# Kernel tuning notes

Measured on AMD Instinct MI355X. Metric: run time of the kernel, lower is better.

Reference implementation:

```python
import jax, jax.numpy as jnp
import numpy as np

# ---- module hyperparameters (init_kwargs) ----
FRAME_PERIOD = 120
SAMPLE_RATE = 24000
FFT_LENGTH = 2048
DEFAULT_F0 = 500.0
Q1 = -0.15
F_MIN = 3.0 * SAMPLE_RATE / (FFT_LENGTH - 3)
EPS_SAFE = 1e-12                      # safeguard noise inside windowing (WORLD kMySafeGuardMinimum)
EPS_F32 = float(np.finfo(np.float32).eps)  # torch.finfo(x.dtype).eps
TAU = 2.0 * np.pi
MAX_F0_STATIC = 600.0                 # static bound on f0 for the smoothing mirror pad
K_PAD = int(MAX_F0_STATIC * 2.0 / 3.0 * FFT_LENGTH / SAMPLE_RATE) + 2

B, T = 8, 120000
N_FRAMES = T // FRAME_PERIOD + 1      # 1001


def setup_inputs() -> dict:
    key = jax.random.key(0)
    kx, kf = jax.random.split(key)
    x = jax.random.normal(kx, (B, T), dtype=jnp.float32)
    # realistic voiced f0 in [100, 400] Hz (always > F_MIN)
    f0 = 100.0 + 300.0 * jax.random.uniform(kf, (B, N_FRAMES), dtype=jnp.float32)
    return {"x": x, "f0": f0}


def _interp_last(c, pos):
    # linear interpolation of c (..., M) at float positions pos (..., K) (interp1Q)
    M = c.shape[-1]
    lo = jnp.clip(jnp.floor(pos).astype(jnp.int32), 0, M - 2)
    frac = pos - lo.astype(pos.dtype)
    c_lo = jnp.take_along_axis(c, lo, axis=-1)
    c_hi = jnp.take_along_axis(c, lo + 1, axis=-1)
    return c_lo + (c_hi - c_lo) * frac


def reference(x, f0):
    L = FFT_LENGTH
    half = L // 2
    K1 = half + 1
    fs = SAMPLE_RATE

    f0 = jnp.where(f0 <= F_MIN, DEFAULT_F0, f0)[..., None]          # (B,N,1)
    f0 = jax.lax.stop_gradient(f0)                                   # .detach() in torch

    # ---- pitch-synchronous Hanning windowing (get_windowed_waveform, ratio=3, bias=0) ----
    n = jnp.arange(f0.shape[1])
    rel = jnp.arange(L) - half                                       # sample offset from frame center
    idx = jnp.clip(n[:, None] * FRAME_PERIOD + rel[None, :], 0, x.shape[-1] - 1)  # (N,L) safe_index
    frames = x[:, idx]                                               # (B,N,L)
    hwl = jnp.round(1.5 * fs / f0)                                   # half window length (B,N,1)
    mask = (jnp.abs(rel) <= hwl).astype(x.dtype)                     # (B,N,L)
    win = (0.5 * jnp.cos(jnp.pi * rel / (1.5 * fs) * f0) + 0.5) * mask
    win = win / jnp.sqrt(jnp.sum(win * win, -1, keepdims=True))      # normalize_power=True
    noise = jax.random.normal(jax.random.key(42), frames.shape, frames.dtype)
    wav = frames * win + EPS_SAFE * noise * mask
    wav = wav - win * (jnp.sum(wav, -1, keepdims=True) / jnp.sum(win, -1, keepdims=True))

    # ---- power spectrum (Spectrum, out_format='power', eps=0) ----
    P = jnp.abs(jnp.fft.rfft(wav, n=L, axis=-1)) ** 2                # (B,N,K1)

    # ---- DC correction: mirror the spectrum around f0 for bins below f0 ----
    k = jnp.arange(K1)
    rate = f0 * L / fs                                               # f0 in bins (B,N,1)
    m = rate - k                                                     # mirror position (B,N,K1)
    lo = jnp.clip(jnp.floor(m).astype(jnp.int32), 0, K1 - 2)
    frac = m - lo.astype(m.dtype)
    repl = jnp.take_along_axis(P, lo, -1) * (1 - frac) + jnp.take_along_axis(P, lo + 1, -1) * frac
    P = P + jnp.where(k < 1 + jnp.floor(rate), repl, 0.0)

    # ---- linear (rectangular) smoothing of width 2/3*f0 Hz via mirrored cumsum ----
    width = f0 * (2.0 / 3.0)                                         # Hz (B,N,1)
    j = jnp.arange(K1 + 2 * K_PAD) - K_PAD
    refl = jnp.abs(j)
    refl = jnp.where(refl > half, L - refl, refl)                    # even reflection at 0 and L/2
    C = jnp.cumsum(P[..., refl] * (fs / L), -1)                      # cumulative integral (B,N,K1+2K)
    wbins = width * L / fs
    pos_lo = k - 0.5 * wbins + (K_PAD - 0.5)                         # grid origin -(K-0.5)*fs/L
    P = (_interp_last(C, pos_lo + wbins) - _interp_last(C, pos_lo)) / width

    # ---- safeguard noise (power_spectrum += |randn| * finfo.eps) ----
    P = P + jnp.abs(jax.random.normal(jax.random.key(43), P.shape, P.dtype)) * EPS_F32

    # ---- cepstral liftering ----
    quef = k / fs                                                    # quefrency axis (K1,)
    z = f0 * quef                                                    # (B,N,K1)
    sl = jnp.sinc(z).at[..., 0].set(1.0)                             # smoothing lifter
    cl = 1 - 2 * Q1 + 2 * Q1 * jnp.cos(TAU * z)                      # compensation lifter
    cep = jnp.fft.irfft(jnp.log(P), n=L, axis=-1)[..., :K1]
    log_power_spectrum = jnp.fft.hfft(cep * sl * cl, axis=-1)[..., :K1]
    return log_power_spectrum
```

## Files before the change

kernel.cpp:

```cpp
#include <hip/hip_runtime.h>
#include <math.h>

#define NFFT   2048
#define N1     1024
#define K1     1025
#define KPAD   36
#define MTOT   1097
#define NFRAMES 1001
#define TLEN   120000
#define BATCH  8
#define FPER   120
#define PIF 3.14159265358979323846f

#define A(i) ((i) ^ (((i) >> 4) & 15))

typedef float2 cpx;
__device__ __forceinline__ cpx cmul(cpx a, cpx b) {
    return make_float2(a.x * b.x - a.y * b.y, a.x * b.y + a.y * b.x);
}
__device__ __forceinline__ cpx cadd(cpx a, cpx b) { return make_float2(a.x + b.x, a.y + b.y); }
__device__ __forceinline__ cpx csub(cpx a, cpx b) { return make_float2(a.x - b.x, a.y - b.y); }

__device__ __forceinline__ int brev10(int v) {
    return (int)(__brev((unsigned)v) >> 22);
}

template<int H>
__device__ __forceinline__ void dif_fused(cpx* c, int tid, cpx w1) {
    int r  = tid & (H / 2 - 1);
    int i0 = (tid / (H / 2)) * (2 * H) + r;
    int ia = A(i0), ib = A(i0 + H / 2), ic = A(i0 + H), id = A(i0 + 3 * H / 2);
    cpx a = c[ia], b = c[ib], cc = c[ic], d = c[id];
    cpx w1n = make_float2(w1.y, -w1.x);
    cpx w2  = make_float2(w1.x * w1.x - w1.y * w1.y, 2.0f * w1.x * w1.y);
    cpx a1 = cadd(a, cc);
    cpx c1 = cmul(csub(a, cc), w1);
    cpx b1 = cadd(b, d);
    cpx d1 = cmul(csub(b, d), w1n);
    c[ia] = cadd(a1, b1);
    c[ib] = cmul(csub(a1, b1), w2);
    c[ic] = cadd(c1, d1);
    c[id] = cmul(csub(c1, d1), w2);
}

__device__ __forceinline__ void dif_last2(cpx* c, int tid) {
    int i0 = 4 * tid;
    int ia = A(i0), ib = A(i0 + 1), ic = A(i0 + 2), id = A(i0 + 3);
    cpx a = c[ia], b = c[ib], cc = c[ic], d = c[id];
    cpx a1 = cadd(a, cc);
    cpx c1 = csub(a, cc);
    cpx b1 = cadd(b, d);
    cpx bd = csub(b, d);
    cpx d1 = make_float2(bd.y, -bd.x);
    c[ia] = cadd(a1, b1);
    c[ib] = csub(a1, b1);
    c[ic] = cadd(c1, d1);
    c[id] = csub(c1, d1);
}

__device__ __forceinline__ void stage1_store(const cpx z[4], cpx* s_c, int tid, cpx w1) {
    cpx w1n = make_float2(w1.y, -w1.x);
    cpx w2  = make_float2(w1.x * w1.x - w1.y * w1.y, 2.0f * w1.x * w1.y);
    cpx a1 = cadd(z[0], z[2]);
    cpx c1 = cmul(csub(z[0], z[2]), w1);
    cpx b1 = cadd(z[1], z[3]);
    cpx d1 = cmul(csub(z[1], z[3]), w1n);
    s_c[A(tid)]       = cadd(a1, b1);
    s_c[A(tid + 256)] = cmul(csub(a1, b1), w2);
    s_c[A(tid + 512)] = cadd(c1, d1);
    s_c[A(tid + 768)] = cmul(csub(c1, d1), w2);
}

__device__ __forceinline__ void fft1024_rest(cpx* c, int tid, const cpx* tw) {
    __syncthreads();
    dif_fused<128>(c, tid, tw[1]);
    dif_fused<32>(c, tid, tw[2]);
    dif_fused<8>(c, tid, tw[3]);
    dif_last2(c, tid);
    __syncthreads();
}

__device__ __forceinline__ void pack_even_stage1(const float* s_P, cpx* s_c,
                                                 int tid, cpx w1) {
    cpx z[4];
#pragma unroll
    for (int c = 0; c < 4; ++c) {
        int m = tid + (c << 8);
        float v0, v1;
        if (c <= 1) {
            v0 = s_P[2 * m]; v1 = s_P[2 * m + 1];
        } else if (m == 512) {
            v0 = s_P[1024]; v1 = s_P[1023];
        } else {
            v0 = s_P[2048 - 2 * m]; v1 = s_P[2047 - 2 * m];
        }
        z[c] = make_float2(v0, v1);
    }
    stage1_store(z, s_c, tid, w1);
}

__device__ __forceinline__ void unpack_pair(const cpx* s_c, int k, cpx w,
                                            cpx& Xk, cpx& Xm) {
    int kk = k & (N1 - 1);
    int mm = (N1 - kk) & (N1 - 1);
    cpx Zk = s_c[A(brev10(kk))];
    cpx Zm = s_c[A(brev10(mm))];
    float Ex = 0.5f * (Zk.x + Zm.x), Ey = 0.5f * (Zk.y - Zm.y);
    float Ox = 0.5f * (Zk.y + Zm.y), Oy = 0.5f * (Zm.x - Zk.x);
    float tx = w.x * Ox - w.y * Oy, ty = w.x * Oy + w.y * Ox;
    Xk = make_float2(Ex + tx, Ey + ty);
    Xm = make_float2(Ex - tx, Ey - ty);
}

__global__ __launch_bounds__(256)
void cheaptrick_kernel(const float* __restrict__ x,
                       const float* __restrict__ f0in,
                       float* __restrict__ out) {
    __shared__ cpx   s_c[1024];
    __shared__ float s_P[1026];
    __shared__ float s_scan[16];
    float* s_C = (float*)s_c;

    const int tid  = threadIdx.x;
    const int lane = tid & 63;
    const int wid  = tid >> 6;
    const int n    = blockIdx.x;
    const int b    = blockIdx.y;

    float f0 = f0in[b * NFRAMES + n];
    const float F_MIN = 72000.0f / 2045.0f;
    if (f0 <= F_MIN) f0 = 500.0f;

    float fr[8], wn[8];
    float hwl = rintf(36000.0f / f0);
    float s_w2 = 0.0f, s_w = 0.0f, s_fw = 0.0f;
    const float* xrow = x + (size_t)b * TLEN;
    int base_idx = n * FPER - N1;
#pragma unroll
    for (int c = 0; c < 4; ++c) {
#pragma unroll
        for (int e = 0; e < 2; ++e) {
            int l = 2 * tid + (c << 9) + e;
            float relf = (float)(l - N1);
            int idx = max(0, min(TLEN - 1, base_idx + l));
            float v = xrow[idx];
            float w = 0.0f;
            if (fabsf(relf) <= hwl) {
                w = 0.5f * __cosf(PIF * relf / 36000.0f * f0) + 0.5f;
            }
            fr[2 * c + e] = v;
            wn[2 * c + e] = w;
            s_w2 += w * w;
            s_w  += w;
            s_fw += v * w;
        }
    }
#pragma unroll
    for (int off = 32; off > 0; off >>= 1) {
        s_w2 += __shfl_down(s_w2, off, 64);
        s_w  += __shfl_down(s_w,  off, 64);
        s_fw += __shfl_down(s_fw, off, 64);
    }
    if (lane == 0) {
        s_scan[wid]     = s_w2;
        s_scan[4 + wid] = s_w;
        s_scan[8 + wid] = s_fw;
    }
    __syncthreads();
    float w2sum = s_scan[0] + s_scan[1] + s_scan[2] + s_scan[3];
    float wsum  = s_scan[4] + s_scan[5] + s_scan[6] + s_scan[7];
    float fwsum = s_scan[8] + s_scan[9] + s_scan[10] + s_scan[11];
    float wscale = 1.0f / sqrtf(w2sum);
    float dc = fwsum / wsum;

    cpx tw[4];
    {
        float sn, cs;
        __sincosf(-PIF * (float)tid * (1.0f / 512.0f), &sn, &cs);
        tw[0] = make_float2(cs, sn);
    }

    {
        cpx z[4];
#pragma unroll
        for (int c = 0; c < 4; ++c) {
            float v0 = wscale * wn[2 * c]     * (fr[2 * c]     - dc);
            float v1 = wscale * wn[2 * c + 1] * (fr[2 * c + 1] - dc);
            z[c] = make_float2(v0, v1);
        }
        stage1_store(z, s_c, tid, tw[0]);
    }

    cpx u2048;
    {
        float sn, cs;
        __sincosf(-PIF * (float)(tid & 63) * (1.0f / 128.0f), &sn, &cs);
        tw[1] = make_float2(cs, sn);
        __sincosf(-PIF * (float)(tid & 15) * (1.0f / 32.0f), &sn, &cs);
        tw[2] = make_float2(cs, sn);
        __sincosf(-PIF * (float)(tid & 3) * (1.0f / 8.0f), &sn, &cs);
        tw[3] = make_float2(cs, sn);
        __sincosf(-PIF * (float)tid * (1.0f / 1024.0f), &sn, &cs);
        u2048 = make_float2(cs, sn);
    }
    const float RH = 0.70710678118654752f;
    const cpx u2048b = cmul(u2048, make_float2(RH, -RH));
    const cpx wmid   = make_float2(0.0f, -1.0f);

    fft1024_rest(s_c, tid, tw);

#pragma unroll
    for (int c2 = 0; c2 < 2; ++c2) {
        int k = tid + (c2 << 8);
        cpx Xk, Xm;
        unpack_pair(s_c, k, (c2 == 0) ? u2048 : u2048b, Xk, Xm);
        s_P[k]        = Xk.x * Xk.x + Xk.y * Xk.y;
        s_P[1024 - k] = Xm.x * Xm.x + Xm.y * Xm.y;
    }
    if (tid == 0) {
        cpx Xk, Xm;
        unpack_pair(s_c, 512, wmid, Xk, Xm);
        s_P[512] = Xk.x * Xk.x + Xk.y * Xk.y;
    }
    __syncthreads();

    float rate = f0 * (2048.0f / 24000.0f);
    int kmax = (int)floorf(rate);
    float repl = 0.0f;
    if (tid <= kmax) {
        float m = rate - (float)tid;
        int lo = (int)floorf(m);
        lo = max(0, min(K1 - 2, lo));
        float frac = m - (float)lo;
        repl = s_P[lo] * (1.0f - frac) + s_P[lo + 1] * frac;
    }
    if (tid <= kmax) s_P[tid] += repl;
    __syncthreads();

    float loc[5];
    float run = 0.0f;
    int basej = tid * 5;
#pragma unroll
    for (int c = 0; c < 5; ++c) {
        int j = basej + c;
        float v = 0.0f;
        if (j < MTOT) {
            int a = abs(j - KPAD);
            if (a > N1) a = NFFT - a;
            v = s_P[a] * (24000.0f / 2048.0f);
        }
        run += v;
        loc[c] = run;
    }
    float v = run;
#pragma unroll
    for (int off = 1; off < 64; off <<= 1) {
        float o = __shfl_up(v, off, 64);
        if (lane >= off) v += o;
    }
    if (lane == 63) s_scan[wid] = v;
    __syncthreads();
    float wbase = 0.0f;
#pragma unroll
    for (int w = 0; w < 4; ++w) wbase += (w < wid) ? s_scan[w] : 0.0f;
    float prefix = wbase + v - run;
#pragma unroll
    for (int c = 0; c < 5; ++c) {
        int j = basej + c;
        if (j < MTOT) s_C[j] = prefix + loc[c];
    }
    __syncthreads();

    float width = f0 * (2.0f / 3.0f);
    float wbins = width * (2048.0f / 24000.0f);
#pragma unroll
    for (int c5 = 0; c5 < 5; ++c5) {
        int k = tid + (c5 << 8);
        if (k < K1) {
            float pos_lo = (float)k - 0.5f * wbins + ((float)KPAD - 0.5f);
            float pos_hi = pos_lo + wbins;
            int llo = (int)floorf(pos_lo); llo = max(0, min(MTOT - 2, llo));
            float flo = pos_lo - (float)llo;
            float clo = s_C[llo] + (s_C[llo + 1] - s_C[llo]) * flo;
            int lhi = (int)floorf(pos_hi); lhi = max(0, min(MTOT - 2, lhi));
            float fhi = pos_hi - (float)lhi;
            float chi = s_C[lhi] + (s_C[lhi + 1] - s_C[lhi]) * fhi;
            s_P[k] = __logf((chi - clo) / width);
        }
    }
    __syncthreads();

    pack_even_stage1(s_P, s_c, tid, tw[0]);
    fft1024_rest(s_c, tid, tw);

#pragma unroll
    for (int c2 = 0; c2 < 2; ++c2) {
        int k = tid + (c2 << 8);
        cpx Xk, Xm;
        unpack_pair(s_c, k, (c2 == 0) ? u2048 : u2048b, Xk, Xm);
        {
            float cep = Xk.x * (1.0f / 2048.0f);
            float pz = PIF * f0 * ((float)k * (1.0f / 24000.0f));
            float s = __sinf(pz);
            float sl = (k != 0) ? (s / pz) : 1.0f;
            s_P[k] = cep * sl * (1.0f + 0.6f * s * s);
        }
        {
            int km = 1024 - k;
            float cep = Xm.x * (1.0f / 2048.0f);
            float pz = PIF * f0 * ((float)km * (1.0f / 24000.0f));
            float s = __sinf(pz);
            s_P[km] = cep * (s / pz) * (1.0f + 0.6f * s * s);
        }
    }
    if (tid == 0) {
        cpx Xk, Xm;
        unpack_pair(s_c, 512, wmid, Xk, Xm);
        float cep = Xk.x * (1.0f / 2048.0f);
        float pz = PIF * f0 * (512.0f / 24000.0f);
        float s = __sinf(pz);
        s_P[512] = cep * (s / pz) * (1.0f + 0.6f * s * s);
    }
    __syncthreads();

    pack_even_stage1(s_P, s_c, tid, tw[0]);
    fft1024_rest(s_c, tid, tw);

    float* orow = out + (size_t)(b * NFRAMES + n) * K1;
#pragma unroll
    for (int c2 = 0; c2 < 2; ++c2) {
        int k = tid + (c2 << 8);
        cpx Xk, Xm;
        unpack_pair(s_c, k, (c2 == 0) ? u2048 : u2048b, Xk, Xm);
        orow[k]        = Xk.x;
        orow[1024 - k] = Xm.x;
    }
    if (tid == 0) {
        cpx Xk, Xm;
        unpack_pair(s_c, 512, wmid, Xk, Xm);
        orow[512] = Xk.x;
    }
}

extern "C" void kernel_launch(void* const* d_in, const int* in_sizes, int n_in,
                              void* d_out, int out_size, void* d_ws, size_t ws_size,
                              hipStream_t stream) {
    (void)in_sizes; (void)n_in; (void)d_ws; (void)ws_size; (void)out_size;
    const float* x  = (const float*)d_in[0];
    const float* f0 = (const float*)d_in[1];
    float* out = (float*)d_out;
    dim3 grid(NFRAMES, BATCH);
    hipLaunchKernelGGL(cheaptrick_kernel, grid, dim3(256), 0, stream, x, f0, out);
}
```

Baseline: 132.9 us.

## Run each frame on a single wavefront with register-resident radix-16 FFT passes

Each frame is now processed by one 64-thread wavefront instead of four, so all __syncthreads barriers and the cross-wave shared-memory reduction disappear. The FFT becomes register-heavy: each thread holds 16 points and does two radix-4 stages in registers between shared-memory exchanges, with new XOR swizzles and a final bit-reversed store so later reads are in natural order. The three FFT passes share one loop, and input loads are vectorised as float2. The trade-offs are much higher register pressure, fewer threads per frame for the serial scan and smoothing loops (19 elements per thread), and reliance on wavefront-synchronous shared-memory ordering with only compiler barriers.

After: 457.0 us. 3.44x slower.

```diff
diff --git a/kernel.cpp b/kernel.cpp
--- a/kernel.cpp
+++ b/kernel.cpp
@@ -12,333 +12,324 @@
 #define FPER   120
 #define PIF 3.14159265358979323846f
 
-#define A(i) ((i) ^ (((i) >> 4) & 15))
 
 typedef float2 cpx;
-__device__ __forceinline__ cpx cmul(cpx a, cpx b) {
-    return make_float2(a.x * b.x - a.y * b.y, a.x * b.y + a.y * b.x);
-}
-__device__ __forceinline__ cpx cadd(cpx a, cpx b) { return make_float2(a.x + b.x, a.y + b.y); }
-__device__ __forceinline__ cpx csub(cpx a, cpx b) { return make_float2(a.x - b.x, a.y - b.y); }
-
-__device__ __forceinline__ int brev10(int v) {
-    return (int)(__brev((unsigned)v) >> 22);
-}
-
-template<int H>
-__device__ __forceinline__ void dif_fused(cpx* c, int tid, cpx w1) {
-    int r  = tid & (H / 2 - 1);
-    int i0 = (tid / (H / 2)) * (2 * H) + r;
-    int ia = A(i0), ib = A(i0 + H / 2), ic = A(i0 + H), id = A(i0 + 3 * H / 2);
-    cpx a = c[ia], b = c[ib], cc = c[ic], d = c[id];
+__device__ __forceinline__ cpx cadd(cpx a, cpx b){ return make_float2(a.x+b.x, a.y+b.y); }
+__device__ __forceinline__ cpx csub(cpx a, cpx b){ return make_float2(a.x-b.x, a.y-b.y); }
+__device__ __forceinline__ cpx cmul(cpx a, cpx b){ return make_float2(a.x*b.x - a.y*b.y, a.x*b.y + a.y*b.x); }
+
+__device__ __forceinline__ int SW(int m){ return m ^ ((m >> 6) & 15); }
+
+__device__ __forceinline__ void bf4(cpx& x0, cpx& x1, cpx& x2, cpx& x3, cpx w1)
+{
     cpx w1n = make_float2(w1.y, -w1.x);
-    cpx w2  = make_float2(w1.x * w1.x - w1.y * w1.y, 2.0f * w1.x * w1.y);
-    cpx a1 = cadd(a, cc);
-    cpx c1 = cmul(csub(a, cc), w1);
-    cpx b1 = cadd(b, d);
-    cpx d1 = cmul(csub(b, d), w1n);
-    c[ia] = cadd(a1, b1);
-    c[ib] = cmul(csub(a1, b1), w2);
-    c[ic] = cadd(c1, d1);
-    c[id] = cmul(csub(c1, d1), w2);
-}
-
-__device__ __forceinline__ void dif_last2(cpx* c, int tid) {
-    int i0 = 4 * tid;
-    int ia = A(i0), ib = A(i0 + 1), ic = A(i0 + 2), id = A(i0 + 3);
-    cpx a = c[ia], b = c[ib], cc = c[ic], d = c[id];
-    cpx a1 = cadd(a, cc);
-    cpx c1 = csub(a, cc);
-    cpx b1 = cadd(b, d);
-    cpx bd = csub(b, d);
+    cpx w2  = make_float2(w1.x*w1.x - w1.y*w1.y, 2.0f*w1.x*w1.y);
+    cpx a1 = cadd(x0, x2);
+    cpx c1 = cmul(csub(x0, x2), w1);
+    cpx b1 = cadd(x1, x3);
+    cpx d1 = cmul(csub(x1, x3), w1n);
+    x0 = cadd(a1, b1);
+    x1 = cmul(csub(a1, b1), w2);
+    x2 = cadd(c1, d1);
+    x3 = cmul(csub(c1, d1), w2);
+}
+__device__ __forceinline__ void bf4_last(cpx& x0, cpx& x1, cpx& x2, cpx& x3)
+{
+    cpx a1 = cadd(x0, x2);
+    cpx c1 = csub(x0, x2);
+    cpx b1 = cadd(x1, x3);
+    cpx bd = csub(x1, x3);
     cpx d1 = make_float2(bd.y, -bd.x);
-    c[ia] = cadd(a1, b1);
-    c[ib] = csub(a1, b1);
-    c[ic] = cadd(c1, d1);
-    c[id] = csub(c1, d1);
-}
-
-__device__ __forceinline__ void stage1_store(const cpx z[4], cpx* s_c, int tid, cpx w1) {
-    cpx w1n = make_float2(w1.y, -w1.x);
-    cpx w2  = make_float2(w1.x * w1.x - w1.y * w1.y, 2.0f * w1.x * w1.y);
-    cpx a1 = cadd(z[0], z[2]);
-    cpx c1 = cmul(csub(z[0], z[2]), w1);
-    cpx b1 = cadd(z[1], z[3]);
-    cpx d1 = cmul(csub(z[1], z[3]), w1n);
-    s_c[A(tid)]       = cadd(a1, b1);
-    s_c[A(tid + 256)] = cmul(csub(a1, b1), w2);
-    s_c[A(tid + 512)] = cadd(c1, d1);
-    s_c[A(tid + 768)] = cmul(csub(c1, d1), w2);
-}
-
-__device__ __forceinline__ void fft1024_rest(cpx* c, int tid, const cpx* tw) {
-    __syncthreads();
-    dif_fused<128>(c, tid, tw[1]);
-    dif_fused<32>(c, tid, tw[2]);
-    dif_fused<8>(c, tid, tw[3]);
-    dif_last2(c, tid);
-    __syncthreads();
-}
-
-__device__ __forceinline__ void pack_even_stage1(const float* s_P, cpx* s_c,
-                                                 int tid, cpx w1) {
-    cpx z[4];
-#pragma unroll
-    for (int c = 0; c < 4; ++c) {
-        int m = tid + (c << 8);
-        float v0, v1;
-        if (c <= 1) {
-            v0 = s_P[2 * m]; v1 = s_P[2 * m + 1];
-        } else if (m == 512) {
-            v0 = s_P[1024]; v1 = s_P[1023];
-        } else {
-            v0 = s_P[2048 - 2 * m]; v1 = s_P[2047 - 2 * m];
-        }
-        z[c] = make_float2(v0, v1);
-    }
-    stage1_store(z, s_c, tid, w1);
-}
-
-__device__ __forceinline__ void unpack_pair(const cpx* s_c, int k, cpx w,
-                                            cpx& Xk, cpx& Xm) {
-    int kk = k & (N1 - 1);
+    x0 = cadd(a1, b1);
+    x1 = csub(a1, b1);
+    x2 = cadd(c1, d1);
+    x3 = csub(c1, d1);
+}
+
+__device__ __forceinline__ void unpack_k(const cpx* s_c, int kk, cpx w,
+                                         cpx& Xk, cpx& Xm)
+{
     int mm = (N1 - kk) & (N1 - 1);
-    cpx Zk = s_c[A(brev10(kk))];
-    cpx Zm = s_c[A(brev10(mm))];
-    float Ex = 0.5f * (Zk.x + Zm.x), Ey = 0.5f * (Zk.y - Zm.y);
-    float Ox = 0.5f * (Zk.y + Zm.y), Oy = 0.5f * (Zm.x - Zk.x);
-    float tx = w.x * Ox - w.y * Oy, ty = w.x * Oy + w.y * Ox;
+    cpx Zk = s_c[SW(kk)];
+    cpx Zm = s_c[SW(mm)];
+    float Ex = 0.5f*(Zk.x + Zm.x), Ey = 0.5f*(Zk.y - Zm.y);
+    float Ox = 0.5f*(Zk.y + Zm.y), Oy = 0.5f*(Zm.x - Zk.x);
+    float tx = w.x*Ox - w.y*Oy, ty = w.x*Oy + w.y*Ox;
     Xk = make_float2(Ex + tx, Ey + ty);
     Xm = make_float2(Ex - tx, Ey - ty);
 }
 
-__global__ __launch_bounds__(256)
+__global__ __launch_bounds__(64, 4)
 void cheaptrick_kernel(const float* __restrict__ x,
                        const float* __restrict__ f0in,
-                       float* __restrict__ out) {
+                       float* __restrict__ out)
+{
     __shared__ cpx   s_c[1024];
     __shared__ float s_P[1026];
-    __shared__ float s_scan[16];
     float* s_C = (float*)s_c;
 
-    const int tid  = threadIdx.x;
-    const int lane = tid & 63;
-    const int wid  = tid >> 6;
-    const int n    = blockIdx.x;
-    const int b    = blockIdx.y;
+    const int t  = threadIdx.x;
+    const int vv = t & 3;
+    const int n  = blockIdx.x;
+    const int b  = blockIdx.y;
 
     float f0 = f0in[b * NFRAMES + n];
     const float F_MIN = 72000.0f / 2045.0f;
     if (f0 <= F_MIN) f0 = 500.0f;
 
-    float fr[8], wn[8];
-    float hwl = rintf(36000.0f / f0);
-    float s_w2 = 0.0f, s_w = 0.0f, s_fw = 0.0f;
-    const float* xrow = x + (size_t)b * TLEN;
-    int base_idx = n * FPER - N1;
-#pragma unroll
-    for (int c = 0; c < 4; ++c) {
-#pragma unroll
-        for (int e = 0; e < 2; ++e) {
-            int l = 2 * tid + (c << 9) + e;
-            float relf = (float)(l - N1);
-            int idx = max(0, min(TLEN - 1, base_idx + l));
-            float v = xrow[idx];
-            float w = 0.0f;
-            if (fabsf(relf) <= hwl) {
-                w = 0.5f * __cosf(PIF * relf / 36000.0f * f0) + 0.5f;
-            }
-            fr[2 * c + e] = v;
-            wn[2 * c + e] = w;
-            s_w2 += w * w;
-            s_w  += w;
-            s_fw += v * w;
+    cpx z[16];
+
+    {
+        const float* xrow = x + (size_t)b * TLEN;
+        const int base_idx = n * FPER - N1;
+        float hwl = rintf(36000.0f / f0);
+        float sw2 = 0.0f, swn = 0.0f, sfw = 0.0f;
+        cpx wn[16];
+#pragma unroll
+        for (int r = 0; r < 16; ++r) {
+            int m  = t + 64 * r;
+            int i0 = base_idx + 2 * m;
+            float v0, v1;
+            if (i0 >= 0 && i0 + 1 <= TLEN - 1) {
+                float2 fv = *reinterpret_cast<const float2*>(xrow + i0);
+                v0 = fv.x; v1 = fv.y;
+            } else {
+                v0 = xrow[max(0, min(TLEN - 1, i0))];
+                v1 = xrow[max(0, min(TLEN - 1, i0 + 1))];
+            }
+            float rel0 = (float)(2 * m - N1);
+            float rel1 = rel0 + 1.0f;
+            float w0 = 0.0f, w1 = 0.0f;
+            if (fabsf(rel0) <= hwl) w0 = 0.5f * __cosf(PIF * rel0 / 36000.0f * f0) + 0.5f;
+            if (fabsf(rel1) <= hwl) w1 = 0.5f * __cosf(PIF * rel1 / 36000.0f * f0) + 0.5f;
+            sw2 += w0 * w0 + w1 * w1;
+            swn += w0 + w1;
+            sfw += v0 * w0 + v1 * w1;
+            z[r]  = make_float2(v0 * w0, v1 * w1);
+            wn[r] = make_float2(w0, w1);
+        }
+#pragma unroll
+        for (int off = 32; off > 0; off >>= 1) {
+            sw2 += __shfl_down(sw2, off, 64);
+            swn += __shfl_down(swn, off, 64);
+            sfw += __shfl_down(sfw, off, 64);
+        }
+        sw2 = __shfl(sw2, 0, 64);
+        swn = __shfl(swn, 0, 64);
+        sfw = __shfl(sfw, 0, 64);
+        float wscale = 1.0f / sqrtf(sw2);
+        float dc = sfw / swn;
+#pragma unroll
+        for (int r = 0; r < 16; ++r) {
+            z[r].x = wscale * (z[r].x - dc * wn[r].x);
+            z[r].y = wscale * (z[r].y - dc * wn[r].y);
         }
     }
-#pragma unroll
-    for (int off = 32; off > 0; off >>= 1) {
-        s_w2 += __shfl_down(s_w2, off, 64);
-        s_w  += __shfl_down(s_w,  off, 64);
-        s_fw += __shfl_down(s_fw, off, 64);
-    }
-    if (lane == 0) {
-        s_scan[wid]     = s_w2;
-        s_scan[4 + wid] = s_w;
-        s_scan[8 + wid] = s_fw;
-    }
-    __syncthreads();
-    float w2sum = s_scan[0] + s_scan[1] + s_scan[2] + s_scan[3];
-    float wsum  = s_scan[4] + s_scan[5] + s_scan[6] + s_scan[7];
-    float fwsum = s_scan[8] + s_scan[9] + s_scan[10] + s_scan[11];
-    float wscale = 1.0f / sqrtf(w2sum);
-    float dc = fwsum / wsum;
-
-    cpx tw[4];
+
+    cpx wA[4], wC[4], wB, wD, wU[8];
     {
         float sn, cs;
-        __sincosf(-PIF * (float)tid * (1.0f / 512.0f), &sn, &cs);
-        tw[0] = make_float2(cs, sn);
+#pragma unroll
+        for (int j = 0; j < 4; ++j) {
+            __sincosf(-PIF * (float)(t + 64 * j) * (1.0f / 512.0f), &sn, &cs);
+            wA[j] = make_float2(cs, sn);
+        }
+        __sincosf(-PIF * (float)t * (1.0f / 128.0f), &sn, &cs);
+        wB = make_float2(cs, sn);
+#pragma unroll
+        for (int a = 0; a < 4; ++a) {
+            __sincosf(-PIF * (float)(4 * a + vv) * (1.0f / 32.0f), &sn, &cs);
+            wC[a] = make_float2(cs, sn);
+        }
+        __sincosf(-PIF * (float)vv * (1.0f / 8.0f), &sn, &cs);
+        wD = make_float2(cs, sn);
+#pragma unroll
+        for (int c = 0; c < 8; ++c) {
+            __sincosf(-PIF * (float)(t + 64 * c) * (1.0f / 1024.0f), &sn, &cs);
+            wU[c] = make_float2(cs, sn);
+        }
     }
-
-    {
-        cpx z[4];
+    const cpx wmid = make_float2(0.0f, -1.0f);
+    const int r6 = (int)(__brev((unsigned)t) >> 26);
+
+#pragma unroll 1
+    for (int pass = 0; pass < 3; ++pass) {
+        if (pass != 0) {
+#pragma unroll
+            for (int r = 0; r < 8; ++r) {
+                int m = t + 64 * r;
+                z[r] = make_float2(s_P[2 * m], s_P[2 * m + 1]);
+            }
+#pragma unroll
+            for (int r = 8; r < 16; ++r) {
+                int m = t + 64 * r;
+                float v0, v1;
+                if (m == 512) { v0 = s_P[1024]; v1 = s_P[1023]; }
+                else          { v0 = s_P[2048 - 2 * m]; v1 = s_P[2047 - 2 * m]; }
+                z[r] = make_float2(v0, v1);
+            }
+        }
+
+#pragma unroll
+        for (int j = 0; j < 4; ++j) bf4(z[j], z[j+4], z[j+8], z[j+12], wA[j]);
+#pragma unroll
+        for (int q = 0; q < 4; ++q) bf4(z[4*q], z[4*q+1], z[4*q+2], z[4*q+3], wB);
+#pragma unroll
+        for (int r = 0; r < 16; ++r) s_c[(t + 64 * r) ^ r] = z[r];
+#pragma unroll
+        for (int u = 0; u < 16; ++u) {
+            int m = 64 * (t >> 2) + 4 * u + vv;
+            z[u] = s_c[m ^ (t >> 2)];
+        }
+#pragma unroll
+        for (int a = 0; a < 4; ++a) bf4(z[a], z[a+4], z[a+8], z[a+12], wC[a]);
+#pragma unroll
+        for (int h = 0; h < 4; ++h) bf4(z[4*h], z[4*h+1], z[4*h+2], z[4*h+3], wD);
+#pragma unroll
+        for (int u = 0; u < 16; ++u) {
+            int m = 64 * (t >> 2) + 4 * u + vv;
+            s_c[m ^ (t >> 2)] = z[u];
+        }
+#pragma unroll
+        for (int c = 0; c < 4; ++c)
+#pragma unroll
+            for (int e = 0; e < 4; ++e) {
+                int m = 4 * t + 256 * c + e;
+                z[4 * c + e] = s_c[SW(m)];
+            }
+#pragma unroll
+        for (int c = 0; c < 4; ++c) bf4_last(z[4*c], z[4*c+1], z[4*c+2], z[4*c+3]);
 #pragma unroll
         for (int c = 0; c < 4; ++c) {
-            float v0 = wscale * wn[2 * c]     * (fr[2 * c]     - dc);
-            float v1 = wscale * wn[2 * c + 1] * (fr[2 * c + 1] - dc);
-            z[c] = make_float2(v0, v1);
-        }
-        stage1_store(z, s_c, tid, tw[0]);
-    }
-
-    cpx u2048;
-    {
-        float sn, cs;
-        __sincosf(-PIF * (float)(tid & 63) * (1.0f / 128.0f), &sn, &cs);
-        tw[1] = make_float2(cs, sn);
-        __sincosf(-PIF * (float)(tid & 15) * (1.0f / 32.0f), &sn, &cs);
-        tw[2] = make_float2(cs, sn);
-        __sincosf(-PIF * (float)(tid & 3) * (1.0f / 8.0f), &sn, &cs);
-        tw[3] = make_float2(cs, sn);
-        __sincosf(-PIF * (float)tid * (1.0f / 1024.0f), &sn, &cs);
-        u2048 = make_float2(cs, sn);
-    }
-    const float RH = 0.70710678118654752f;
-    const cpx u2048b = cmul(u2048, make_float2(RH, -RH));
-    const cpx wmid   = make_float2(0.0f, -1.0f);
-
-    fft1024_rest(s_c, tid, tw);
-
-#pragma unroll
-    for (int c2 = 0; c2 < 2; ++c2) {
-        int k = tid + (c2 << 8);
-        cpx Xk, Xm;
-        unpack_pair(s_c, k, (c2 == 0) ? u2048 : u2048b, Xk, Xm);
-        s_P[k]        = Xk.x * Xk.x + Xk.y * Xk.y;
-        s_P[1024 - k] = Xm.x * Xm.x + Xm.y * Xm.y;
-    }
-    if (tid == 0) {
-        cpx Xk, Xm;
-        unpack_pair(s_c, 512, wmid, Xk, Xm);
-        s_P[512] = Xk.x * Xk.x + Xk.y * Xk.y;
-    }
-    __syncthreads();
-
-    float rate = f0 * (2048.0f / 24000.0f);
-    int kmax = (int)floorf(rate);
-    float repl = 0.0f;
-    if (tid <= kmax) {
-        float m = rate - (float)tid;
-        int lo = (int)floorf(m);
-        lo = max(0, min(K1 - 2, lo));
-        float frac = m - (float)lo;
-        repl = s_P[lo] * (1.0f - frac) + s_P[lo + 1] * frac;
-    }
-    if (tid <= kmax) s_P[tid] += repl;
-    __syncthreads();
-
-    float loc[5];
-    float run = 0.0f;
-    int basej = tid * 5;
-#pragma unroll
-    for (int c = 0; c < 5; ++c) {
-        int j = basej + c;
-        float v = 0.0f;
-        if (j < MTOT) {
-            int a = abs(j - KPAD);
-            if (a > N1) a = NFFT - a;
-            v = s_P[a] * (24000.0f / 2048.0f);
-        }
-        run += v;
-        loc[c] = run;
-    }
-    float v = run;
-#pragma unroll
-    for (int off = 1; off < 64; off <<= 1) {
-        float o = __shfl_up(v, off, 64);
-        if (lane >= off) v += o;
-    }
-    if (lane == 63) s_scan[wid] = v;
-    __syncthreads();
-    float wbase = 0.0f;
-#pragma unroll
-    for (int w = 0; w < 4; ++w) wbase += (w < wid) ? s_scan[w] : 0.0f;
-    float prefix = wbase + v - run;
-#pragma unroll
-    for (int c = 0; c < 5; ++c) {
-        int j = basej + c;
-        if (j < MTOT) s_C[j] = prefix + loc[c];
-    }
-    __syncthreads();
-
-    float width = f0 * (2.0f / 3.0f);
-    float wbins = width * (2048.0f / 24000.0f);
-#pragma unroll
-    for (int c5 = 0; c5 < 5; ++c5) {
-        int k = tid + (c5 << 8);
-        if (k < K1) {
-            float pos_lo = (float)k - 0.5f * wbins + ((float)KPAD - 0.5f);
-            float pos_hi = pos_lo + wbins;
-            int llo = (int)floorf(pos_lo); llo = max(0, min(MTOT - 2, llo));
-            float flo = pos_lo - (float)llo;
-            float clo = s_C[llo] + (s_C[llo + 1] - s_C[llo]) * flo;
-            int lhi = (int)floorf(pos_hi); lhi = max(0, min(MTOT - 2, lhi));
-            float fhi = pos_hi - (float)lhi;
-            float chi = s_C[lhi] + (s_C[lhi + 1] - s_C[lhi]) * fhi;
-            s_P[k] = __logf((chi - clo) / width);
-        }
-    }
-    __syncthreads();
-
-    pack_even_stage1(s_P, s_c, tid, tw[0]);
-    fft1024_rest(s_c, tid, tw);
-
-#pragma unroll
-    for (int c2 = 0; c2 < 2; ++c2) {
-        int k = tid + (c2 << 8);
-        cpx Xk, Xm;
-        unpack_pair(s_c, k, (c2 == 0) ? u2048 : u2048b, Xk, Xm);
-        {
-            float cep = Xk.x * (1.0f / 2048.0f);
-            float pz = PIF * f0 * ((float)k * (1.0f / 24000.0f));
-            float s = __sinf(pz);
-            float sl = (k != 0) ? (s / pz) : 1.0f;
-            s_P[k] = cep * sl * (1.0f + 0.6f * s * s);
-        }
-        {
-            int km = 1024 - k;
-            float cep = Xm.x * (1.0f / 2048.0f);
-            float pz = PIF * f0 * ((float)km * (1.0f / 24000.0f));
-            float s = __sinf(pz);
-            s_P[km] = cep * (s / pz) * (1.0f + 0.6f * s * s);
-        }
-    }
-    if (tid == 0) {
-        cpx Xk, Xm;
-        unpack_pair(s_c, 512, wmid, Xk, Xm);
-        float cep = Xk.x * (1.0f / 2048.0f);
-        float pz = PIF * f0 * (512.0f / 24000.0f);
-        float s = __sinf(pz);
-        s_P[512] = cep * (s / pz) * (1.0f + 0.6f * s * s);
-    }
-    __syncthreads();
-
-    pack_even_stage1(s_P, s_c, tid, tw[0]);
-    fft1024_rest(s_c, tid, tw);
-
-    float* orow = out + (size_t)(b * NFRAMES + n) * K1;
-#pragma unroll
-    for (int c2 = 0; c2 < 2; ++c2) {
-        int k = tid + (c2 << 8);
-        cpx Xk, Xm;
-        unpack_pair(s_c, k, (c2 == 0) ? u2048 : u2048b, Xk, Xm);
-        orow[k]        = Xk.x;
-        orow[1024 - k] = Xm.x;
-    }
-    if (tid == 0) {
-        cpx Xk, Xm;
-        unpack_pair(s_c, 512, wmid, Xk, Xm);
-        orow[512] = Xk.x;
+            int rc = ((c & 1) << 1) | (c >> 1);
+#pragma unroll
+            for (int e = 0; e < 4; ++e) {
+                int re = ((e & 1) << 1) | (e >> 1);
+                int k = (re << 8) | (r6 << 2) | rc;
+                s_c[SW(k)] = z[4 * c + e];
+            }
+        }
+
+        if (pass == 0) {
+#pragma unroll
+            for (int c = 0; c < 8; ++c) {
+                int kk = t + 64 * c;
+                cpx Xk, Xm;
+                unpack_k(s_c, kk, wU[c], Xk, Xm);
+                s_P[kk]        = Xk.x * Xk.x + Xk.y * Xk.y;
+                s_P[1024 - kk] = Xm.x * Xm.x + Xm.y * Xm.y;
+            }
+            if (t == 0) {
+                cpx Xk, Xm;
+                unpack_k(s_c, 512, wmid, Xk, Xm);
+                s_P[512] = Xk.x * Xk.x + Xk.y * Xk.y;
+            }
+
+            float rate = f0 * (2048.0f / 24000.0f);
+            int kmax = (int)floorf(rate);
+            if (t <= kmax) {
+                float m = rate - (float)t;
+                int lo = (int)floorf(m);
+                lo = max(0, min(K1 - 2, lo));
+                float frac = m - (float)lo;
+                float repl = s_P[lo] * (1.0f - frac) + s_P[lo + 1] * frac;
+                s_P[t] += repl;
+            }
+
+            asm volatile("" ::: "memory");
+
+            float loc[19];
+            float run = 0.0f;
+            const int basej = t * 19;
+#pragma unroll
+            for (int c = 0; c < 19; ++c) {
+                int j = basej + c;
+                float v = 0.0f;
+                if (j < MTOT) {
+                    int a = abs(j - KPAD);
+                    if (a > N1) a = NFFT - a;
+                    v = s_P[a] * (24000.0f / 2048.0f);
+                }
+                run += v;
+                loc[c] = run;
+            }
+            float sv = run;
+#pragma unroll
+            for (int off = 1; off < 64; off <<= 1) {
+                float o = __shfl_up(sv, off, 64);
+                if (t >= off) sv += o;
+            }
+            float prefix = sv - run;
+#pragma unroll
+            for (int c = 0; c < 19; ++c) {
+                int j = basej + c;
+                if (j < MTOT) s_C[j] = prefix + loc[c];
+            }
+
+            float width = f0 * (2.0f / 3.0f);
+            float wbins = width * (2048.0f / 24000.0f);
+#pragma unroll
+            for (int c = 0; c < 17; ++c) {
+                int k = t + 64 * c;
+                if (k < K1) {
+                    float pos_lo = (float)k - 0.5f * wbins + ((float)KPAD - 0.5f);
+                    float pos_hi = pos_lo + wbins;
+                    int llo = (int)floorf(pos_lo); llo = max(0, min(MTOT - 2, llo));
+                    float flo = pos_lo - (float)llo;
+                    float clo = s_C[llo] + (s_C[llo + 1] - s_C[llo]) * flo;
+                    int lhi = (int)floorf(pos_hi); lhi = max(0, min(MTOT - 2, lhi));
+                    float fhi = pos_hi - (float)lhi;
+                    float chi = s_C[lhi] + (s_C[lhi + 1] - s_C[lhi]) * fhi;
+                    s_P[k] = __logf((chi - clo) / width);
+                }
+            }
+
+            asm volatile("" ::: "memory");
+        } else if (pass == 1) {
+#pragma unroll
+            for (int c = 0; c < 8; ++c) {
+                int kk = t + 64 * c;
+                cpx Xk, Xm;
+                unpack_k(s_c, kk, wU[c], Xk, Xm);
+                {
+                    float cep = Xk.x * (1.0f / 2048.0f);
+                    float pz = PIF * f0 * ((float)kk * (1.0f / 24000.0f));
+                    float s = __sinf(pz);
+                    float sl = (kk != 0) ? (s / pz) : 1.0f;
+                    s_P[kk] = cep * sl * (1.0f + 0.6f * s * s);
+                }
+                {
+                    int km = 1024 - kk;
+                    float cep = Xm.x * (1.0f / 2048.0f);
+                    float pz = PIF * f0 * ((float)km * (1.0f / 24000.0f));
+                    float s = __sinf(pz);
+                    s_P[km] = cep * (s / pz) * (1.0f + 0.6f * s * s);
+                }
+            }
+            if (t == 0) {
+                cpx Xk, Xm;
+                unpack_k(s_c, 512, wmid, Xk, Xm);
+                float cep = Xk.x * (1.0f / 2048.0f);
+                float pz = PIF * f0 * (512.0f / 24000.0f);
+                float s = __sinf(pz);
+                s_P[512] = cep * (s / pz) * (1.0f + 0.6f * s * s);
+            }
+        } else {
+            float* orow = out + (size_t)(b * NFRAMES + n) * K1;
+#pragma unroll
+            for (int c = 0; c < 8; ++c) {
+                int kk = t + 64 * c;
+                cpx Xk, Xm;
+                unpack_k(s_c, kk, wU[c], Xk, Xm);
+                orow[kk]        = Xk.x;
+                orow[1024 - kk] = Xm.x;
+            }
+            if (t == 0) {
+                cpx Xk, Xm;
+                unpack_k(s_c, 512, wmid, Xk, Xm);
+                orow[512] = Xk.x;
+            }
+        }
     }
 }
 
@@ -350,5 +341,5 @@
     const float* f0 = (const float*)d_in[1];
     float* out = (float*)d_out;
     dim3 grid(NFRAMES, BATCH);
-    hipLaunchKernelGGL(cheaptrick_kernel, grid, dim3(256), 0, stream, x, f0, out);
-}
+    hipLaunchKernelGGL(cheaptrick_kernel, grid, dim3(64), 0, stream, x, f0, out);
+}
```
